# Performance work log

Measured on AMD Instinct MI355X. Metric: run time of the kernel, lower is better.

Reference implementation:

```python
import jax, jax.numpy as jnp
import numpy as np

N_EMBD = 384
HEAD_SIZE = 64
B, T = 512, 256


def setup_inputs() -> dict:
    key = jax.random.key(0)
    ks = jax.random.split(key, 7)
    s = 1.0 / np.sqrt(N_EMBD)  # torch Linear default init scale
    return {
        "x": jax.random.normal(ks[0], (B, T, N_EMBD), dtype=jnp.float32),
        "Wq": jax.random.uniform(ks[1], (N_EMBD, HEAD_SIZE), jnp.float32, -s, s),
        "bq": jax.random.uniform(ks[2], (HEAD_SIZE,), jnp.float32, -s, s),
        "Wk": jax.random.uniform(ks[3], (N_EMBD, HEAD_SIZE), jnp.float32, -s, s),
        "bk": jax.random.uniform(ks[4], (HEAD_SIZE,), jnp.float32, -s, s),
        "Wv": jax.random.uniform(ks[5], (N_EMBD, HEAD_SIZE), jnp.float32, -s, s),
        "bv": jax.random.uniform(ks[6], (HEAD_SIZE,), jnp.float32, -s, s),
    }


def reference(x, Wq, bq, Wk, bk, Wv, bv):
    # Single causal self-attention head (nanoGPT 'Head', eval mode: dropout = identity)
    q = x @ Wq + bq  # [B, T, H]
    k = x @ Wk + bk
    v = x @ Wv + bv
    Tq = x.shape[1]
    scale = x.shape[-1] ** -0.5  # NOTE: source scales by n_embd (C), not head_size
    wei = jnp.einsum("btd,bsd->bts", q, k) * scale  # [B, T, T]
    mask = jnp.tril(jnp.ones((Tq, Tq), dtype=bool))
    wei = jnp.where(mask, wei, -jnp.inf)
    wei = jax.nn.softmax(wei, axis=-1)
    return jnp.einsum("bts,bsd->btd", wei, v)  # [B, T, H]
```

## Files before the change

kernel.cpp:

```cpp
#include <hip/hip_runtime.h>
#include <hip/hip_bf16.h>


#define Bsz 512
#define Tt  256
#define Cc  384
#define Hh  64

typedef __attribute__((ext_vector_type(8))) short bf16x8;
typedef __attribute__((ext_vector_type(4))) float f32x4;

__device__ __forceinline__ unsigned short f2bf(float f) {
    unsigned int u = __float_as_uint(f);
    unsigned int r = (u + 0x7fffu + ((u >> 16) & 1u)) >> 16;
    return (unsigned short)r;
}
__device__ __forceinline__ float bf2f(unsigned short b) {
    return __uint_as_float(((unsigned int)b) << 16);
}

__global__ __launch_bounds__(256) void prep_kernel(const float* __restrict__ Wq,
                                                   const float* __restrict__ Wk,
                                                   const float* __restrict__ Wv,
                                                   unsigned short* __restrict__ wt) {
    int idx = blockIdx.x * 256 + threadIdx.x;
    if (idx >= 192 * 384) return;
    int n = idx / 384, k = idx - n * 384;
    const float* W = (n < 64) ? Wq : ((n < 128) ? Wk : Wv);
    wt[n * 384 + k] = f2bf(W[k * 64 + (n & 63)]);
}

__global__ __launch_bounds__(256) void qkv_kernel(const float* __restrict__ x,
                                                  const float* __restrict__ bq,
                                                  const float* __restrict__ bk,
                                                  const float* __restrict__ bv,
                                                  const unsigned short* __restrict__ wt,
                                                  unsigned short* __restrict__ qws,
                                                  unsigned short* __restrict__ kws,
                                                  unsigned short* __restrict__ vws) {
    __shared__ unsigned short xl[128 * 40];
    __shared__ unsigned short wl[192 * 40];

    const int w = threadIdx.x >> 6;
    const int lane = threadIdx.x & 63;
    const int quad = lane >> 4;
    const int cl = lane & 15;
    const int rb = blockIdx.x * 128;

    f32x4 acc[2][12];
    for (int rt = 0; rt < 2; ++rt)
        for (int nt = 0; nt < 12; ++nt) acc[rt][nt] = (f32x4){0.f, 0.f, 0.f, 0.f};

    for (int ks = 0; ks < 12; ++ks) {
        const int k0 = ks * 32;
        for (int l = threadIdx.x; l < 1024; l += 256) {
            int row = l >> 3, off = (l & 7) << 2;
            float4 xv = *(const float4*)(x + (size_t)(rb + row) * Cc + k0 + off);
            unsigned long long pk = (unsigned long long)f2bf(xv.x)
                                  | ((unsigned long long)f2bf(xv.y) << 16)
                                  | ((unsigned long long)f2bf(xv.z) << 32)
                                  | ((unsigned long long)f2bf(xv.w) << 48);
            *(unsigned long long*)&xl[row * 40 + off] = pk;
        }
        for (int l = threadIdx.x; l < 768; l += 256) {
            int row = l >> 2, off = (l & 3) << 3;
            uint4 wv = *(const uint4*)(wt + (size_t)row * Cc + k0 + off);
            *(uint4*)&wl[row * 40 + off] = wv;
        }
        __syncthreads();

        bf16x8 a0 = *(const bf16x8*)&xl[(w * 32 + cl) * 40 + quad * 8];
        bf16x8 a1 = *(const bf16x8*)&xl[(w * 32 + 16 + cl) * 40 + quad * 8];
        for (int nt = 0; nt < 12; ++nt) {
            bf16x8 bfr = *(const bf16x8*)&wl[(nt * 16 + cl) * 40 + quad * 8];
            acc[0][nt] = __builtin_amdgcn_mfma_f32_16x16x32_bf16(a0, bfr, acc[0][nt], 0, 0, 0);
            acc[1][nt] = __builtin_amdgcn_mfma_f32_16x16x32_bf16(a1, bfr, acc[1][nt], 0, 0, 0);
        }
        __syncthreads();
    }

    for (int nt = 0; nt < 12; ++nt) {
        int col = nt * 16 + cl;
        float bias = (col < 64) ? bq[col] : ((col < 128) ? bk[col - 64] : bv[col - 128]);
        unsigned short* wsout = (col < 64) ? qws : ((col < 128) ? kws : vws);
        int h = col & 63;
        for (int rt = 0; rt < 2; ++rt)
            for (int r = 0; r < 4; ++r) {
                int m = rb + w * 32 + rt * 16 + quad * 4 + r;
                wsout[(size_t)m * Hh + h] = f2bf(acc[rt][nt][r] + bias);
            }
    }
}

__global__ __launch_bounds__(256) void attn_kernel(const unsigned short* __restrict__ qws,
                                                   const unsigned short* __restrict__ kws,
                                                   const unsigned short* __restrict__ vws,
                                                   float* __restrict__ out) {
    __shared__ unsigned short Kl[128 * 72];
    __shared__ unsigned short Vt[64 * 136];
    __shared__ unsigned short Ql[64 * 72];
    __shared__ unsigned short Pl[4 * 16 * 136];

    const int w = threadIdx.x >> 6;
    const int lane = threadIdx.x & 63;
    const int quad = lane >> 4;
    const int cl = lane & 15;
    const int qbase = blockIdx.x * 64;
    const int bb = blockIdx.y;
    const int qrow0 = qbase + w * 16;
    const float SL2E = 0.07362224f;

    for (int l = threadIdx.x; l < 512; l += 256) {
        int row = l >> 3, off = (l & 7) << 3;
        uint4 v = *(const uint4*)(qws + ((size_t)(bb * Tt + qbase + row)) * Hh + off);
        *(uint4*)&Ql[row * 72 + off] = v;
    }

    f32x4 o[4];
    for (int ht = 0; ht < 4; ++ht) o[ht] = (f32x4){0.f, 0.f, 0.f, 0.f};
    float rs[4] = {0.f, 0.f, 0.f, 0.f};

    const int nchunk = (qbase + 191) >> 7;
    for (int c = 0; c < nchunk; ++c) {
        const int kbase = c * 128;
        for (int l = threadIdx.x; l < 1024; l += 256) {
            int row = l >> 3, off = (l & 7) << 3;
            uint4 v = *(const uint4*)(kws + ((size_t)(bb * Tt + kbase + row)) * Hh + off);
            *(uint4*)&Kl[row * 72 + off] = v;
        }
        for (int l = threadIdx.x; l < 1024; l += 256) {
            int s = l >> 3, h0 = (l & 7) << 3;
            uint4 v = *(const uint4*)(vws + ((size_t)(bb * Tt + kbase + s)) * Hh + h0);
            const unsigned short* e = (const unsigned short*)&v;
            for (int j = 0; j < 8; ++j) Vt[(h0 + j) * 136 + s] = e[j];
        }
        __syncthreads();

        bf16x8 aq0 = *(const bf16x8*)&Ql[(w * 16 + cl) * 72 + quad * 8];
        bf16x8 aq1 = *(const bf16x8*)&Ql[(w * 16 + cl) * 72 + 32 + quad * 8];

        const int qlast = qrow0 + 15;
        const int kt = min(8, ((qlast - kbase) >> 4) + 1);
        const int ktr = (kt + 1) & ~1;

        for (int ct = 0; ct < kt; ++ct) {
            f32x4 sc = (f32x4){0.f, 0.f, 0.f, 0.f};
            bf16x8 b0 = *(const bf16x8*)&Kl[(ct * 16 + cl) * 72 + quad * 8];
            bf16x8 b1 = *(const bf16x8*)&Kl[(ct * 16 + cl) * 72 + 32 + quad * 8];
            sc = __builtin_amdgcn_mfma_f32_16x16x32_bf16(aq0, b0, sc, 0, 0, 0);
            sc = __builtin_amdgcn_mfma_f32_16x16x32_bf16(aq1, b1, sc, 0, 0, 0);
            int key = kbase + ct * 16 + cl;
            for (int r = 0; r < 4; ++r) {
                int qg = qrow0 + quad * 4 + r;
                float p = 0.f;
                if (key <= qg) p = exp2f(sc[r] * SL2E);
                unsigned short pb = f2bf(p);
                rs[r] += bf2f(pb);
                Pl[(w * 16 + quad * 4 + r) * 136 + ct * 16 + cl] = pb;
            }
        }
        for (int ct = kt; ct < ktr; ++ct)
            for (int r = 0; r < 4; ++r)
                Pl[(w * 16 + quad * 4 + r) * 136 + ct * 16 + cl] = 0;
        __syncthreads();

        for (int ks2 = 0; ks2 < (ktr >> 1); ++ks2) {
            bf16x8 ap = *(const bf16x8*)&Pl[(w * 16 + cl) * 136 + ks2 * 32 + quad * 8];
            for (int ht = 0; ht < 4; ++ht) {
                bf16x8 bvf = *(const bf16x8*)&Vt[(ht * 16 + cl) * 136 + ks2 * 32 + quad * 8];
                o[ht] = __builtin_amdgcn_mfma_f32_16x16x32_bf16(ap, bvf, o[ht], 0, 0, 0);
            }
        }
        __syncthreads();
    }

    for (int r = 0; r < 4; ++r) {
        float s = rs[r];
        s += __shfl_xor(s, 1);
        s += __shfl_xor(s, 2);
        s += __shfl_xor(s, 4);
        s += __shfl_xor(s, 8);
        float inv = 1.0f / s;
        int t = qrow0 + quad * 4 + r;
        for (int ht = 0; ht < 4; ++ht)
            out[((size_t)(bb * Tt + t)) * Hh + ht * 16 + cl] = o[ht][r] * inv;
    }
}

extern "C" void kernel_launch(void* const* d_in, const int* in_sizes, int n_in,
                              void* d_out, int out_size, void* d_ws, size_t ws_size,
                              hipStream_t stream) {
    const float* x  = (const float*)d_in[0];
    const float* Wq = (const float*)d_in[1];
    const float* bq = (const float*)d_in[2];
    const float* Wk = (const float*)d_in[3];
    const float* bk = (const float*)d_in[4];
    const float* Wv = (const float*)d_in[5];
    const float* bv = (const float*)d_in[6];
    float* out = (float*)d_out;

    char* ws = (char*)d_ws;
    unsigned short* wt  = (unsigned short*)(ws);
    unsigned short* qws = (unsigned short*)(ws + (size_t)(1  << 20));
    unsigned short* kws = (unsigned short*)(ws + (size_t)(17 << 20));
    unsigned short* vws = (unsigned short*)(ws + (size_t)(33 << 20));

    prep_kernel<<<288, 256, 0, stream>>>(Wq, Wk, Wv, wt);
    qkv_kernel<<<1024, 256, 0, stream>>>(x, bq, bk, bv, wt, qws, kws, vws);
    attn_kernel<<<dim3(4, Bsz), 256, 0, stream>>>(qws, kws, vws, out);
}
```

Baseline: 392.8 us.

## Load QKV GEMM operands straight from global memory and drop redundant attention barriers

```diff
diff --git a/kernel.cpp b/kernel.cpp
--- a/kernel.cpp
+++ b/kernel.cpp
@@ -17,6 +17,14 @@
 }
 __device__ __forceinline__ float bf2f(unsigned short b) {
     return __uint_as_float(((unsigned int)b) << 16);
+}
+__device__ __forceinline__ bf16x8 pack8(float4 a, float4 b) {
+    bf16x8 r;
+    r[0] = (short)f2bf(a.x); r[1] = (short)f2bf(a.y);
+    r[2] = (short)f2bf(a.z); r[3] = (short)f2bf(a.w);
+    r[4] = (short)f2bf(b.x); r[5] = (short)f2bf(b.y);
+    r[6] = (short)f2bf(b.z); r[7] = (short)f2bf(b.w);
+    return r;
 }
 
 __global__ __launch_bounds__(256) void prep_kernel(const float* __restrict__ Wq,
@@ -30,53 +38,42 @@
     wt[n * 384 + k] = f2bf(W[k * 64 + (n & 63)]);
 }
 
-__global__ __launch_bounds__(256) void qkv_kernel(const float* __restrict__ x,
-                                                  const float* __restrict__ bq,
-                                                  const float* __restrict__ bk,
-                                                  const float* __restrict__ bv,
-                                                  const unsigned short* __restrict__ wt,
-                                                  unsigned short* __restrict__ qws,
-                                                  unsigned short* __restrict__ kws,
-                                                  unsigned short* __restrict__ vws) {
-    __shared__ unsigned short xl[128 * 40];
-    __shared__ unsigned short wl[192 * 40];
-
+__global__ __launch_bounds__(256, 2) void qkv_kernel(const float* __restrict__ x,
+                                                     const float* __restrict__ bq,
+                                                     const float* __restrict__ bk,
+                                                     const float* __restrict__ bv,
+                                                     const unsigned short* __restrict__ wt,
+                                                     unsigned short* __restrict__ qws,
+                                                     unsigned short* __restrict__ kws,
+                                                     unsigned short* __restrict__ vws) {
     const int w = threadIdx.x >> 6;
     const int lane = threadIdx.x & 63;
     const int quad = lane >> 4;
     const int cl = lane & 15;
-    const int rb = blockIdx.x * 128;
+    const int rb = blockIdx.x * 128 + w * 32;
 
     f32x4 acc[2][12];
     for (int rt = 0; rt < 2; ++rt)
         for (int nt = 0; nt < 12; ++nt) acc[rt][nt] = (f32x4){0.f, 0.f, 0.f, 0.f};
 
+    const float* xr0 = x + (size_t)(rb + cl) * Cc;
+    const float* xr1 = x + (size_t)(rb + 16 + cl) * Cc;
+    const unsigned short* wrow = wt + (size_t)cl * Cc + quad * 8;
+
     for (int ks = 0; ks < 12; ++ks) {
-        const int k0 = ks * 32;
-        for (int l = threadIdx.x; l < 1024; l += 256) {
-            int row = l >> 3, off = (l & 7) << 2;
-            float4 xv = *(const float4*)(x + (size_t)(rb + row) * Cc + k0 + off);
-            unsigned long long pk = (unsigned long long)f2bf(xv.x)
-                                  | ((unsigned long long)f2bf(xv.y) << 16)
-                                  | ((unsigned long long)f2bf(xv.z) << 32)
-                                  | ((unsigned long long)f2bf(xv.w) << 48);
-            *(unsigned long long*)&xl[row * 40 + off] = pk;
-        }
-        for (int l = threadIdx.x; l < 768; l += 256) {
-            int row = l >> 2, off = (l & 3) << 3;
-            uint4 wv = *(const uint4*)(wt + (size_t)row * Cc + k0 + off);
-            *(uint4*)&wl[row * 40 + off] = wv;
-        }
-        __syncthreads();
-
-        bf16x8 a0 = *(const bf16x8*)&xl[(w * 32 + cl) * 40 + quad * 8];
-        bf16x8 a1 = *(const bf16x8*)&xl[(w * 32 + 16 + cl) * 40 + quad * 8];
+        const int k0 = ks * 32 + quad * 8;
+        float4 xa = *(const float4*)(xr0 + k0);
+        float4 xb = *(const float4*)(xr0 + k0 + 4);
+        float4 xc = *(const float4*)(xr1 + k0);
+        float4 xd = *(const float4*)(xr1 + k0 + 4);
+        bf16x8 a0 = pack8(xa, xb);
+        bf16x8 a1 = pack8(xc, xd);
+#pragma unroll
         for (int nt = 0; nt < 12; ++nt) {
-            bf16x8 bfr = *(const bf16x8*)&wl[(nt * 16 + cl) * 40 + quad * 8];
+            bf16x8 bfr = *(const bf16x8*)(wrow + (size_t)nt * 16 * Cc + ks * 32);
             acc[0][nt] = __builtin_amdgcn_mfma_f32_16x16x32_bf16(a0, bfr, acc[0][nt], 0, 0, 0);
             acc[1][nt] = __builtin_amdgcn_mfma_f32_16x16x32_bf16(a1, bfr, acc[1][nt], 0, 0, 0);
         }
-        __syncthreads();
     }
 
     for (int nt = 0; nt < 12; ++nt) {
@@ -86,7 +83,7 @@
         int h = col & 63;
         for (int rt = 0; rt < 2; ++rt)
             for (int r = 0; r < 4; ++r) {
-                int m = rb + w * 32 + rt * 16 + quad * 4 + r;
+                int m = rb + rt * 16 + quad * 4 + r;
                 wsout[(size_t)m * Hh + h] = f2bf(acc[rt][nt][r] + bias);
             }
     }
@@ -162,7 +159,8 @@
         for (int ct = kt; ct < ktr; ++ct)
             for (int r = 0; r < 4; ++r)
                 Pl[(w * 16 + quad * 4 + r) * 136 + ct * 16 + cl] = 0;
-        __syncthreads();
+
+        asm volatile("s_waitcnt lgkmcnt(0)" ::: "memory");
 
         for (int ks2 = 0; ks2 < (ktr >> 1); ++ks2) {
             bf16x8 ap = *(const bf16x8*)&Pl[(w * 16 + cl) * 136 + ks2 * 32 + quad * 8];
@@ -171,7 +169,7 @@
                 o[ht] = __builtin_amdgcn_mfma_f32_16x16x32_bf16(ap, bvf, o[ht], 0, 0, 0);
             }
         }
-        __syncthreads();
+        if (c + 1 < nchunk) __syncthreads();
     }
 
     for (int r = 0; r < 4; ++r) {
```

New measurement: 388.4 us. No clear change (-1.1%).
